# Performance work log

Measured on AMD Instinct MI355X. Metric: run time of the kernel, lower is better.

The kernel has to match this reference:

```python
import jax, jax.numpy as jnp
import numpy as np

DIM = 384
K = 64               # num_classes
TEMP = 0.1
BASE_TEMP = 2.0
LAMB = 25.0
PIXEL_SIZE = 50      # pixel_update_freq * 5
K_BAN = 10
SINKHORN_ITERS = 3
BS, N = 16, 512


def _l2norm(x, eps=1e-12):
    return x / jnp.maximum(jnp.linalg.norm(x, axis=-1, keepdims=True), eps)


def _online_clustering(scores):
    # SwAV-style Sinkhorn in log space on lamb-scaled cosine logits, then argmax.
    logq = scores
    for _ in range(SINKHORN_ITERS):
        logq = logq - jax.scipy.special.logsumexp(logq, axis=1, keepdims=True)
        logq = logq - jax.scipy.special.logsumexp(logq, axis=0, keepdims=True)
    return jnp.argmax(logq, axis=1)


def _supcon(anchor, y_anchor, contrast, y_contrast, exclude_diag, require_pos):
    # mask[i,j] = 1 if same label
    mask = (y_anchor[:, None] == y_contrast[None, :]).astype(anchor.dtype)
    logits = (anchor @ contrast.T) / TEMP
    logits = logits - jax.lax.stop_gradient(jnp.max(logits, axis=1, keepdims=True))
    if exclude_diag:
        mask = mask * (1.0 - jnp.eye(anchor.shape[0], dtype=anchor.dtype))
    exp_logits = jnp.exp(logits)
    # note: neg_mask = 1 - mask, so for exclude_diag the self term counts as negative (faithful)
    neg = (exp_logits * (1.0 - mask)).sum(axis=1, keepdims=True)
    log_prob = logits - jnp.log(exp_logits + neg)
    pos_cnt = mask.sum(axis=1)
    num = (mask * log_prob).sum(axis=1)
    if require_pos:
        valid = (pos_cnt > 0).astype(anchor.dtype)
        mlpp = jnp.where(pos_cnt > 0, num / jnp.maximum(pos_cnt, 1.0), 0.0)
        return -(TEMP / BASE_TEMP) * jnp.sum(mlpp) / jnp.maximum(valid.sum(), 1.0)
    return jnp.mean(-(TEMP / BASE_TEMP) * num / pos_cnt)


def _forward(feats, off_feats, cluster_center, point_queue):
    bs, n, dim = off_feats.shape
    n_off = _l2norm(off_feats.reshape(-1, dim))
    cluster_feats = jnp.concatenate([n_off, point_queue.reshape(-1, dim)], axis=0)
    log_alpha = cluster_feats @ cluster_center.T              # (bs*n + K*PIXEL_SIZE, K)
    labels = _online_clustering(log_alpha * LAMB)[: bs * n]
    f = _l2norm(feats).reshape(-1, dim)
    # ppc2: anchors vs sampled queue entries (same random column indices for every class)
    k_samp = PIXEL_SIZE - K_BAN
    idx = jax.random.permutation(jax.random.key(1), PIXEL_SIZE)[:k_samp]
    x_c = point_queue[:, idx, :].reshape(-1, dim)             # (K*k_samp, dim)
    y_c = jnp.repeat(jnp.arange(K), k_samp)
    loss = _supcon(f, labels, x_c, y_c, exclude_diag=False, require_pos=False)
    # ppc: anchors vs anchors, diagonal removed from positives
    loss = loss + _supcon(f, labels, f, labels, exclude_diag=True, require_pos=True)
    return loss


def setup_inputs() -> dict:
    key = jax.random.key(0)
    k1, k2, k3, k4 = jax.random.split(key, 4)
    feats = jax.random.normal(k1, (BS, N, DIM), dtype=jnp.float32)
    off_feats = jax.random.normal(k2, (BS, N, DIM), dtype=jnp.float32)
    cluster_center = _l2norm(jax.random.normal(k3, (K, DIM), dtype=jnp.float32))
    point_queue = _l2norm(jax.random.normal(k4, (K, PIXEL_SIZE, DIM), dtype=jnp.float32))
    return {"feats": feats, "off_feats": off_feats,
            "cluster_center": cluster_center, "point_queue": point_queue}


def reference(feats, off_feats, cluster_center, point_queue):
    return _forward(feats, off_feats, cluster_center, point_queue)
```

## Files before the change

### kernel.cpp

```cpp
#include <hip/hip_runtime.h>
#include <stdint.h>
#include <algorithm>

#define DIM   384
#define KCLS  64
#define NPIX  50
#define KSAMP 40
#define NANCH 8192
#define NQ    3200
#define NTOT  11392
#define NXC   2560

typedef __attribute__((ext_vector_type(8)))  short s16x8;
typedef __attribute__((ext_vector_type(16))) float f32x16;

struct Idx40 { int v[KSAMP]; };

__device__ __forceinline__ float wave_sum64(float v){
  #pragma unroll
  for (int o = 32; o >= 1; o >>= 1) v += __shfl_xor(v, o);
  return v;
}

__device__ __forceinline__ unsigned short f2bf(float x){
  union { float f; uint32_t u; } c; c.f = x;
  uint32_t r = c.u + 0x7FFFu + ((c.u >> 16) & 1u);
  if ((c.u & 0x7F800000u) == 0x7F800000u) r = c.u;
  return (unsigned short)(r >> 16);
}

__device__ __forceinline__ float bf2f(unsigned short h){
  union { uint32_t u; float f; } c; c.u = ((uint32_t)h) << 16;
  return c.f;
}

__device__ __forceinline__ void split_hl(float x, unsigned short& hi, unsigned short& lo){
  hi = f2bf(x);
  lo = f2bf(x - bf2f(hi));
}

__device__ __forceinline__ void gload16(const unsigned short* g, unsigned short* l){
  __builtin_amdgcn_global_load_lds(
      (const __attribute__((address_space(1))) unsigned int*)g,
      (__attribute__((address_space(3))) unsigned int*)l, 16, 0, 0);
}

__global__ __launch_bounds__(256) void norm_copy_k(const float* __restrict__ feats,
    const float* __restrict__ off, const float* __restrict__ pq,
    const float* __restrict__ CC,
    unsigned short* __restrict__ fNh,
    unsigned short* __restrict__ CFhi, unsigned short* __restrict__ CFlo,
    unsigned short* __restrict__ cchi, unsigned short* __restrict__ cclo,
    unsigned short* __restrict__ xch, Idx40 idx){
  int row  = blockIdx.x * 4 + (threadIdx.x >> 6);
  int lane = threadIdx.x & 63;
  if (row < 2 * NANCH){
    const float* src = (row < NANCH) ? feats + (size_t)row * DIM
                                     : off + (size_t)(row - NANCH) * DIM;
    float v[6]; float ss = 0.f;
    #pragma unroll
    for (int e = 0; e < 6; e++){ v[e] = src[lane + 64 * e]; ss += v[e] * v[e]; }
    ss = wave_sum64(ss);
    float inv = 1.f / fmaxf(sqrtf(ss), 1e-12f);
    if (row < NANCH){
      unsigned short* dh = fNh + (size_t)row * DIM;
      #pragma unroll
      for (int e = 0; e < 6; e++) dh[lane + 64 * e] = f2bf(v[e] * inv);
    } else {
      size_t base = (size_t)(row - NANCH) * DIM;
      #pragma unroll
      for (int e = 0; e < 6; e++){
        unsigned short h, l;
        split_hl(v[e] * inv, h, l);
        CFhi[base + lane + 64 * e] = h;
        CFlo[base + lane + 64 * e] = l;
      }
    }
  } else if (row < 2 * NANCH + NQ){
    int q = row - 2 * NANCH;
    const float* src = pq + (size_t)q * DIM;
    size_t base = (size_t)(NANCH + q) * DIM;
    #pragma unroll
    for (int e = 0; e < 6; e++){
      unsigned short h, l;
      split_hl(src[lane + 64 * e], h, l);
      CFhi[base + lane + 64 * e] = h;
      CFlo[base + lane + 64 * e] = l;
    }
  } else if (row < 2 * NANCH + NQ + KCLS){
    int r = row - 2 * NANCH - NQ;
    size_t base = (size_t)r * DIM;
    #pragma unroll
    for (int e = 0; e < 6; e++){
      unsigned short h, l;
      split_hl(CC[base + lane + 64 * e], h, l);
      cchi[base + lane + 64 * e] = h;
      cclo[base + lane + 64 * e] = l;
    }
  } else {
    int q = row - 2 * NANCH - NQ - KCLS;
    int c = q / KSAMP, t = q - c * KSAMP;
    const float* src = pq + ((size_t)c * NPIX + idx.v[t]) * DIM;
    unsigned short* dst = xch + (size_t)q * DIM;
    #pragma unroll
    for (int e = 0; e < 6; e++) dst[lane + 64 * e] = f2bf(src[lane + 64 * e]);
  }
}

__global__ __launch_bounds__(256) void gemm_logq_mfma_k(
    const unsigned short* __restrict__ Ahi, const unsigned short* __restrict__ Alo,
    const unsigned short* __restrict__ Bhi, const unsigned short* __restrict__ Blo,
    float* __restrict__ logq){
  __shared__ unsigned short lAh[128 * 64], lAl[128 * 64];
  __shared__ unsigned short lBh[64 * 64],  lBl[64 * 64];
  int t = threadIdx.x;
  int lane = t & 63, w = t >> 6;
  int l31 = lane & 31, half = lane >> 5;
  int i0 = blockIdx.x * 128;

  int rA = w * 32 + l31;
  int swA = ((rA & 7) << 4);
  int rB0 = l31, rB1 = 32 + l31;
  int swB = ((l31 & 7) << 4);

  f32x16 acc0, acc1;
  #pragma unroll
  for (int r = 0; r < 16; r++){ acc0[r] = 0.f; acc1[r] = 0.f; }

  for (int kc = 0; kc < 6; kc++){
    __syncthreads();
    #pragma unroll
    for (int p = 0; p < 4; p++){
      int c = t + p * 256;
      int row = c >> 3, col = c & 7;
      int sw = ((col << 4) ^ ((row & 7) << 4));
      *(s16x8*)((char*)lAh + row * 128 + sw) =
          *(const s16x8*)(Ahi + (size_t)(i0 + row) * DIM + kc * 64 + col * 8);
      *(s16x8*)((char*)lAl + row * 128 + sw) =
          *(const s16x8*)(Alo + (size_t)(i0 + row) * DIM + kc * 64 + col * 8);
    }
    #pragma unroll
    for (int p = 0; p < 2; p++){
      int c = t + p * 256;
      int row = c >> 3, col = c & 7;
      int sw = ((col << 4) ^ ((row & 7) << 4));
      *(s16x8*)((char*)lBh + row * 128 + sw) =
          *(const s16x8*)(Bhi + (size_t)row * DIM + kc * 64 + col * 8);
      *(s16x8*)((char*)lBl + row * 128 + sw) =
          *(const s16x8*)(Blo + (size_t)row * DIM + kc * 64 + col * 8);
    }
    __syncthreads();
    #pragma unroll
    for (int kk = 0; kk < 4; kk++){
      int kb = kk * 32 + half * 16;
      s16x8 fah  = *(const s16x8*)((char*)lAh + rA * 128 + (kb ^ swA));
      s16x8 fal  = *(const s16x8*)((char*)lAl + rA * 128 + (kb ^ swA));
      s16x8 fb0h = *(const s16x8*)((char*)lBh + rB0 * 128 + (kb ^ swB));
      s16x8 fb0l = *(const s16x8*)((char*)lBl + rB0 * 128 + (kb ^ swB));
      s16x8 fb1h = *(const s16x8*)((char*)lBh + rB1 * 128 + (kb ^ swB));
      s16x8 fb1l = *(const s16x8*)((char*)lBl + rB1 * 128 + (kb ^ swB));
      acc0 = __builtin_amdgcn_mfma_f32_32x32x16_bf16(fah, fb0h, acc0, 0, 0, 0);
      acc0 = __builtin_amdgcn_mfma_f32_32x32x16_bf16(fah, fb0l, acc0, 0, 0, 0);
      acc0 = __builtin_amdgcn_mfma_f32_32x32x16_bf16(fal, fb0h, acc0, 0, 0, 0);
      acc1 = __builtin_amdgcn_mfma_f32_32x32x16_bf16(fah, fb1h, acc1, 0, 0, 0);
      acc1 = __builtin_amdgcn_mfma_f32_32x32x16_bf16(fah, fb1l, acc1, 0, 0, 0);
      acc1 = __builtin_amdgcn_mfma_f32_32x32x16_bf16(fal, fb1h, acc1, 0, 0, 0);
    }
  }
  #pragma unroll
  for (int r = 0; r < 16; r++){
    int rowp = (r & 3) + 8 * (r >> 2) + 4 * half;
    size_t row = (size_t)(i0 + w * 32 + rowp);
    logq[row * KCLS + l31]      = 25.f * acc0[r];
    logq[row * KCLS + 32 + l31] = 25.f * acc1[r];
  }
}

__global__ __launch_bounds__(256) void rowpass_k(float* __restrict__ logq,
    const float* __restrict__ colsum, int useCol){
  int row  = blockIdx.x * 4 + (threadIdx.x >> 6);
  int lane = threadIdx.x & 63;
  float v = logq[(size_t)row * KCLS + lane];
  if (useCol) v -= logf(colsum[lane]);
  float m = v;
  #pragma unroll
  for (int o = 32; o >= 1; o >>= 1) m = fmaxf(m, __shfl_xor(m, o));
  float s = expf(v - m);
  s = wave_sum64(s);
  logq[(size_t)row * KCLS + lane] = v - (m + logf(s));
}

__global__ __launch_bounds__(256) void colsum_k(const float* __restrict__ logq,
    float* __restrict__ cs){
  int r0 = blockIdx.x * 128;
  int t = threadIdx.x, lane = t & 63, grp = t >> 6;
  float acc = 0.f;
  for (int r = grp; r < 128; r += 4)
    acc += __expf(logq[(size_t)(r0 + r) * KCLS + lane]);
  __shared__ float red[4][64];
  red[grp][lane] = acc;
  __syncthreads();
  if (t < 64) atomicAdd(&cs[t], red[0][t] + red[1][t] + red[2][t] + red[3][t]);
}

__global__ __launch_bounds__(256) void argmax_k(const float* __restrict__ logq,
    const float* __restrict__ cs, int* __restrict__ labels, int* __restrict__ cnt){
  __shared__ float clog[KCLS];
  int t = threadIdx.x;
  if (t < KCLS) clog[t] = logf(cs[t]);
  __syncthreads();
  int i = blockIdx.x * 256 + t;
  if (i >= NANCH) return;
  float best = -INFINITY; int bj = 0;
  for (int j = 0; j < KCLS; j++){
    float v = logq[(size_t)i * KCLS + j] - clog[j];
    if (v > best){ best = v; bj = j; }
  }
  labels[i] = bj;
  atomicAdd(&cnt[bj], 1);
}

__global__ void scan_k(const int* cnt, int* offs, int* offw){
  if (threadIdx.x == 0){
    int acc = 0;
    for (int c = 0; c < KCLS; c++){ offs[c] = acc; offw[c] = acc; acc += cnt[c]; }
  }
}

__global__ __launch_bounds__(256) void scatter_k(const int* __restrict__ labels,
    int* offw, int* __restrict__ sorted, const float* __restrict__ S,
    const float* __restrict__ S2, float* __restrict__ Sp, float* __restrict__ S2p){
  int i = blockIdx.x * 256 + threadIdx.x;
  if (i >= NANCH) return;
  int p = atomicAdd(&offw[labels[i]], 1);
  sorted[p] = i;
  Sp[p]  = S[i];
  S2p[p] = S2[i];
}

__global__ __launch_bounds__(256) void sortrows_k(const unsigned short* __restrict__ fNh,
    const int* __restrict__ sorted, unsigned short* __restrict__ fNs){
  int p = blockIdx.x * 4 + (threadIdx.x >> 6);
  int lane = threadIdx.x & 63;
  int src = sorted[p];
  const uint32_t* s = (const uint32_t*)(fNh + (size_t)src * DIM);
  uint32_t* d = (uint32_t*)(fNs + (size_t)p * DIM);
  #pragma unroll
  for (int e = 0; e < 3; e++) d[lane + 64 * e] = s[lane + 64 * e];
}

__global__ __launch_bounds__(256) void rowsums2_k(
    const unsigned short* __restrict__ A, const unsigned short* __restrict__ Bself,
    const unsigned short* __restrict__ Bxc, float* __restrict__ S, float* __restrict__ S2){
  __shared__ unsigned short lds[2][2][128 * 64];
  const unsigned short* Bp; float* dst; int jbase;
  if (blockIdx.y < 16){ Bp = Bself; dst = S;  jbase = blockIdx.y * 512; }
  else                { Bp = Bxc;   dst = S2; jbase = (blockIdx.y - 16) * 512; }

  int t = threadIdx.x, lane = t & 63, w = t >> 6;
  int wr = w >> 1, wc = w & 1;
  int l31 = lane & 31, half = lane >> 5;
  int i0 = blockIdx.x * 128;
  int lrow = lane >> 3, srcslot = (lane & 7) ^ lrow;
  size_t loff = (size_t)lrow * DIM + srcslot * 8;

  int rA0 = wr * 64 + l31, rA1 = rA0 + 32;
  int rB0 = wc * 64 + l31, rB1 = rB0 + 32;
  int swA = ((rA0 & 7) << 4), swB = ((rB0 & 7) << 4);

  f32x16 s0, s1, a00, a01, a10, a11;
  #pragma unroll
  for (int r = 0; r < 16; r++){ s0[r] = 0.f; s1[r] = 0.f; }

  #pragma unroll
  for (int c = 0; c < 4; c++){
    int chunk = w * 4 + c;
    gload16(A  + (size_t)(i0    + chunk * 8) * DIM + loff, &lds[0][0][chunk * 512]);
    gload16(Bp + (size_t)(jbase + chunk * 8) * DIM + loff, &lds[0][1][chunk * 512]);
  }
  __syncthreads();

  int buf = 0;
  for (int s = 0; s < 24; s++){
    int kc = s % 6;
    if (s < 23){
      int sn = s + 1;
      int jt1 = sn / 6, kc1 = sn - jt1 * 6;
      int j0 = jbase + jt1 * 128;
      int nb = buf ^ 1;
      #pragma unroll
      for (int c = 0; c < 4; c++){
        int chunk = w * 4 + c;
        gload16(A  + (size_t)(i0 + chunk * 8) * DIM + kc1 * 64 + loff, &lds[nb][0][chunk * 512]);
        gload16(Bp + (size_t)(j0 + chunk * 8) * DIM + kc1 * 64 + loff, &lds[nb][1][chunk * 512]);
      }
    }
    if (kc == 0){
      #pragma unroll
      for (int r = 0; r < 16; r++){ a00[r] = 0.f; a01[r] = 0.f; a10[r] = 0.f; a11[r] = 0.f; }
    }
    const char* bA = (const char*)&lds[buf][0][0];
    const char* bB = (const char*)&lds[buf][1][0];
    #pragma unroll
    for (int kk = 0; kk < 4; kk++){
      int kb = kk * 32 + half * 16;
      s16x8 fa0 = *(const s16x8*)(bA + rA0 * 128 + (kb ^ swA));
      s16x8 fa1 = *(const s16x8*)(bA + rA1 * 128 + (kb ^ swA));
      s16x8 fb0 = *(const s16x8*)(bB + rB0 * 128 + (kb ^ swB));
      s16x8 fb1 = *(const s16x8*)(bB + rB1 * 128 + (kb ^ swB));
      a00 = __builtin_amdgcn_mfma_f32_32x32x16_bf16(fa0, fb0, a00, 0, 0, 0);
      a01 = __builtin_amdgcn_mfma_f32_32x32x16_bf16(fa0, fb1, a01, 0, 0, 0);
      a10 = __builtin_amdgcn_mfma_f32_32x32x16_bf16(fa1, fb0, a10, 0, 0, 0);
      a11 = __builtin_amdgcn_mfma_f32_32x32x16_bf16(fa1, fb1, a11, 0, 0, 0);
    }
    if (kc == 5){
      #pragma unroll
      for (int r = 0; r < 16; r++){
        s0[r] += __expf(fmaf(a00[r], 10.f, -10.f)) + __expf(fmaf(a01[r], 10.f, -10.f));
        s1[r] += __expf(fmaf(a10[r], 10.f, -10.f)) + __expf(fmaf(a11[r], 10.f, -10.f));
      }
    }
    __syncthreads();
    buf ^= 1;
  }

  #pragma unroll
  for (int o = 1; o < 32; o <<= 1){
    #pragma unroll
    for (int r = 0; r < 16; r++){
      s0[r] += __shfl_xor(s0[r], o);
      s1[r] += __shfl_xor(s1[r], o);
    }
  }
  if (l31 == 0){
    #pragma unroll
    for (int r = 0; r < 16; r++){
      int rowp = (r & 3) + 8 * (r >> 2) + 4 * half;
      atomicAdd(&dst[i0 + wr * 64 + rowp], s0[r]);
      atomicAdd(&dst[i0 + wr * 64 + 32 + rowp], s1[r]);
    }
  }
}

__device__ __forceinline__ void gram2(const s16x8* afr,
    const unsigned short* b0, const unsigned short* b1, f32x16& acc0, f32x16& acc1){
  #pragma unroll
  for (int ks = 0; ks < 24; ks++){
    s16x8 v0 = *(const s16x8*)(b0 + ks * 16);
    s16x8 v1 = *(const s16x8*)(b1 + ks * 16);
    acc0 = __builtin_amdgcn_mfma_f32_32x32x16_bf16(afr[ks], v0, acc0, 0, 0, 0);
    acc1 = __builtin_amdgcn_mfma_f32_32x32x16_bf16(afr[ks], v1, acc1, 0, 0, 0);
  }
}

__global__ __launch_bounds__(64) void classpair_k(
    const unsigned short* __restrict__ fNs, const unsigned short* __restrict__ xch,
    const int* __restrict__ offs, const int* __restrict__ cnt,
    const float* __restrict__ S, const float* __restrict__ S2,
    float* __restrict__ num2A, float* __restrict__ mlppA, float* __restrict__ validA){
  int c = blockIdx.x;
  int n = cnt[c], o0 = offs[c];
  if (n == 0) return;
  int lane = threadIdx.x;
  int l31 = lane & 31, half = lane >> 5;
  int ntiles = (n + 31) >> 5;

  for (int rt = blockIdx.y; rt < ntiles; rt += gridDim.y){
    int rpos = rt * 32 + l31;
    const unsigned short* arow = fNs + (size_t)(o0 + (rpos < n ? rpos : 0)) * DIM + half * 8;
    s16x8 afr[24];
    #pragma unroll
    for (int ks = 0; ks < 24; ks++) afr[ks] = *(const s16x8*)(arow + ks * 16);

    f32x16 p20, p21;
    #pragma unroll
    for (int r = 0; r < 16; r++){ p20[r] = 0.f; p21[r] = 0.f; }
    {
      int c1 = 32 + l31;
      const unsigned short* b0 = xch + ((size_t)c * KSAMP + l31) * DIM + half * 8;
      const unsigned short* b1 = xch + ((size_t)c * KSAMP + (c1 < KSAMP ? c1 : 0)) * DIM + half * 8;
      gram2(afr, b0, b1, p20, p21);
    }
    f32x16 red;
    #pragma unroll
    for (int r = 0; r < 16; r++){
      float v0 = expf(fmaf(p20[r], 10.f, -10.f));
      float v1 = (l31 < 8) ? expf(fmaf(p21[r], 10.f, -10.f)) : 0.f;
      red[r] = v0 + v1;
    }
    #pragma unroll
    for (int o = 1; o < 32; o <<= 1)
      #pragma unroll
      for (int r = 0; r < 16; r++) red[r] += __shfl_xor(red[r], o);
    float neg2[16];
    #pragma unroll
    for (int r = 0; r < 16; r++){
      int rowp = (r & 3) + 8 * (r >> 2) + 4 * half;
      int rp = rt * 32 + rowp;
      neg2[r] = (rp < n) ? S2[o0 + rp] - red[r] : 1.f;
    }
    #pragma unroll
    for (int r = 0; r < 16; r++){
      float l0 = fmaf(p20[r], 10.f, -10.f);
      float l1 = fmaf(p21[r], 10.f, -10.f);
      float a = l0 - logf(expf(l0) + neg2[r]);
      float b = (l31 < 8) ? l1 - logf(expf(l1) + neg2[r]) : 0.f;
      red[r] = a + b;
    }
    #pragma unroll
    for (int o = 1; o < 32; o <<= 1)
      #pragma unroll
      for (int r = 0; r < 16; r++) red[r] += __shfl_xor(red[r], o);
    if (l31 == 0){
      #pragma unroll
      for (int r = 0; r < 16; r++){
        int rowp = (r & 3) + 8 * (r >> 2) + 4 * half;
        int rp = rt * 32 + rowp;
        if (rp < n) num2A[o0 + rp] = red[r];
      }
    }

    f32x16 pe;
    #pragma unroll
    for (int r = 0; r < 16; r++) pe[r] = 0.f;
    for (int ct = 0; ct < ntiles; ct += 2){
      int cp0 = ct * 32 + l31;
      int cp1 = (ct + 1) * 32 + l31;
      bool has1 = (ct + 1) < ntiles;
      const unsigned short* b0 = fNs + (size_t)(o0 + (cp0 < n ? cp0 : 0)) * DIM + half * 8;
      const unsigned short* b1 = fNs + (size_t)(o0 + (has1 && cp1 < n ? cp1 : 0)) * DIM + half * 8;
      f32x16 a0, a1;
      #pragma unroll
      for (int r = 0; r < 16; r++){ a0[r] = 0.f; a1[r] = 0.f; }
      gram2(afr, b0, b1, a0, a1);
      #pragma unroll
      for (int r = 0; r < 16; r++){
        int rowp = (r & 3) + 8 * (r >> 2) + 4 * half;
        int rp = rt * 32 + rowp;
        if (cp0 < n && cp0 != rp) pe[r] += expf(fmaf(a0[r], 10.f, -10.f));
        if (has1 && cp1 < n && cp1 != rp) pe[r] += expf(fmaf(a1[r], 10.f, -10.f));
      }
    }
    #pragma unroll
    for (int o = 1; o < 32; o <<= 1)
      #pragma unroll
      for (int r = 0; r < 16; r++) pe[r] += __shfl_xor(pe[r], o);
    float neg[16];
    #pragma unroll
    for (int r = 0; r < 16; r++){
      int rowp = (r & 3) + 8 * (r >> 2) + 4 * half;
      int rp = rt * 32 + rowp;
      neg[r] = (rp < n) ? S[o0 + rp] - pe[r] : 1.f;
    }

    f32x16 nm;
    #pragma unroll
    for (int r = 0; r < 16; r++) nm[r] = 0.f;
    for (int ct = 0; ct < ntiles; ct += 2){
      int cp0 = ct * 32 + l31;
      int cp1 = (ct + 1) * 32 + l31;
      bool has1 = (ct + 1) < ntiles;
      const unsigned short* b0 = fNs + (size_t)(o0 + (cp0 < n ? cp0 : 0)) * DIM + half * 8;
      const unsigned short* b1 = fNs + (size_t)(o0 + (has1 && cp1 < n ? cp1 : 0)) * DIM + half * 8;
      f32x16 a0, a1;
      #pragma unroll
      for (int r = 0; r < 16; r++){ a0[r] = 0.f; a1[r] = 0.f; }
      gram2(afr, b0, b1, a0, a1);
      #pragma unroll
      for (int r = 0; r < 16; r++){
        int rowp = (r & 3) + 8 * (r >> 2) + 4 * half;
        int rp = rt * 32 + rowp;
        if (cp0 < n && cp0 != rp){
          float l = fmaf(a0[r], 10.f, -10.f);
          nm[r] += l - logf(expf(l) + neg[r]);
        }
        if (has1 && cp1 < n && cp1 != rp){
          float l = fmaf(a1[r], 10.f, -10.f);
          nm[r] += l - logf(expf(l) + neg[r]);
        }
      }
    }
    #pragma unroll
    for (int o = 1; o < 32; o <<= 1)
      #pragma unroll
      for (int r = 0; r < 16; r++) nm[r] += __shfl_xor(nm[r], o);
    if (l31 == 0){
      #pragma unroll
      for (int r = 0; r < 16; r++){
        int rowp = (r & 3) + 8 * (r >> 2) + 4 * half;
        int rp = rt * 32 + rowp;
        if (rp < n){
          if (n > 1){ mlppA[o0 + rp] = nm[r] / (float)(n - 1); validA[o0 + rp] = 1.f; }
          else      { mlppA[o0 + rp] = 0.f; validA[o0 + rp] = 0.f; }
        }
      }
    }
  }
}

__global__ __launch_bounds__(256) void finalize_k(const float* __restrict__ num2A,
    const float* __restrict__ mlppA, const float* __restrict__ validA,
    float* __restrict__ out){
  int t = threadIdx.x;
  float s2 = 0.f, sm = 0.f, sv = 0.f;
  for (int i = t; i < NANCH; i += 256){ s2 += num2A[i]; sm += mlppA[i]; sv += validA[i]; }
  __shared__ float a2[256], am[256], av[256];
  a2[t] = s2; am[t] = sm; av[t] = sv; __syncthreads();
  for (int o = 128; o >= 1; o >>= 1){
    if (t < o){ a2[t] += a2[t+o]; am[t] += am[t+o]; av[t] += av[t+o]; }
    __syncthreads();
  }
  if (t == 0){
    float loss1 = -0.05f * a2[0] / (40.f * (float)NANCH);
    float loss2 = -0.05f * am[0] / fmaxf(av[0], 1.f);
    out[0] = loss1 + loss2;
  }
}

static void tf2x32(uint32_t k0, uint32_t k1, uint32_t x0, uint32_t x1, uint32_t out[2]){
  uint32_t ks[3] = { k0, k1, k0 ^ k1 ^ 0x1BD11BDAu };
  static const int R[2][4] = { {13,15,26,6}, {17,29,16,24} };
  x0 += ks[0]; x1 += ks[1];
  for (int i = 0; i < 5; i++){
    for (int j = 0; j < 4; j++){
      x0 += x1;
      int r = R[i & 1][j];
      x1 = (x1 << r) | (x1 >> (32 - r));
      x1 ^= x0;
    }
    x0 += ks[(i + 1) % 3];
    x1 += ks[(i + 2) % 3] + (uint32_t)(i + 1);
  }
  out[0] = x0; out[1] = x1;
}

static void compute_idx(int idx_out[KSAMP]){
  uint32_t p0[2], p1[2];
  tf2x32(0u, 1u, 0u, 2u, p0);
  tf2x32(0u, 1u, 1u, 3u, p1);
  uint32_t sk0 = p0[1], sk1 = p1[1];
  uint32_t bits[NPIX];
  for (int i = 0; i < 25; i++){
    uint32_t o[2];
    tf2x32(sk0, sk1, (uint32_t)i, (uint32_t)(25 + i), o);
    bits[i] = o[0]; bits[25 + i] = o[1];
  }
  int perm[NPIX];
  for (int i = 0; i < NPIX; i++) perm[i] = i;
  std::stable_sort(perm, perm + NPIX, [&](int a, int b){ return bits[a] < bits[b]; });
  for (int i = 0; i < KSAMP; i++) idx_out[i] = perm[i];
}

extern "C" void kernel_launch(void* const* d_in, const int* in_sizes, int n_in,
                              void* d_out, int out_size, void* d_ws, size_t ws_size,
                              hipStream_t stream){
  const float* feats = (const float*)d_in[0];
  const float* off   = (const float*)d_in[1];
  const float* cc    = (const float*)d_in[2];
  const float* pq    = (const float*)d_in[3];
  float* out = (float*)d_out;

  char* ws = (char*)d_ws;
  size_t ofs = 0;
  auto alloc = [&](size_t bytes) -> void* {
    ofs = (ofs + 255) & ~(size_t)255;
    void* p = ws + ofs;
    ofs += bytes;
    return p;
  };
  float* logq   = (float*)alloc((size_t)NTOT * KCLS * 4);
  unsigned short* fNh  = (unsigned short*)alloc((size_t)NANCH * DIM * 2);
  unsigned short* fNs  = (unsigned short*)alloc((size_t)NANCH * DIM * 2);
  unsigned short* CFhi = (unsigned short*)alloc((size_t)NTOT * DIM * 2);
  unsigned short* CFlo = (unsigned short*)alloc((size_t)NTOT * DIM * 2);
  unsigned short* cchi = (unsigned short*)alloc((size_t)KCLS * DIM * 2);
  unsigned short* cclo = (unsigned short*)alloc((size_t)KCLS * DIM * 2);
  unsigned short* xch  = (unsigned short*)alloc((size_t)NXC * DIM * 2);
  float* S2     = (float*)alloc((2 * NANCH + KCLS + 3 * KCLS) * 4);
  float* S      = S2 + NANCH;
  int*   cnt    = (int*)(S2 + 2 * NANCH);
  float* cs0    = S2 + 2 * NANCH + KCLS;
  float* cs1    = cs0 + KCLS;
  float* cs2    = cs1 + KCLS;
  float* Sp     = (float*)alloc(NANCH * 4);
  float* S2p    = (float*)alloc(NANCH * 4);
  float* num2A  = (float*)alloc(NANCH * 4);
  float* mlppA  = (float*)alloc(NANCH * 4);
  float* validA = (float*)alloc(NANCH * 4);
  int* labels   = (int*)alloc(NANCH * 4);
  int* sorted   = (int*)alloc(NANCH * 4);
  int* offs     = (int*)alloc(KCLS * 4);
  int* offw     = (int*)alloc(KCLS * 4);

  Idx40 idx;
  compute_idx(idx.v);

  hipMemsetAsync(S2, 0, (2 * NANCH + 4 * KCLS) * 4, stream);
  norm_copy_k<<<(2 * NANCH + NQ + KCLS + NXC) / 4, 256, 0, stream>>>(
      feats, off, pq, cc, fNh, CFhi, CFlo, cchi, cclo, xch, idx);
  rowsums2_k<<<dim3(64, 21), 256, 0, stream>>>(fNh, fNh, xch, S, S2);
  gemm_logq_mfma_k<<<NTOT / 128, 256, 0, stream>>>(CFhi, CFlo, cchi, cclo, logq);
  rowpass_k<<<NTOT / 4, 256, 0, stream>>>(logq, cs0, 0);
  colsum_k<<<NTOT / 128, 256, 0, stream>>>(logq, cs0);
  rowpass_k<<<NTOT / 4, 256, 0, stream>>>(logq, cs0, 1);
  colsum_k<<<NTOT / 128, 256, 0, stream>>>(logq, cs1);
  rowpass_k<<<NTOT / 4, 256, 0, stream>>>(logq, cs1, 1);
  colsum_k<<<NTOT / 128, 256, 0, stream>>>(logq, cs2);
  argmax_k<<<NANCH / 256, 256, 0, stream>>>(logq, cs2, labels, cnt);
  scan_k<<<1, 64, 0, stream>>>(cnt, offs, offw);
  scatter_k<<<NANCH / 256, 256, 0, stream>>>(labels, offw, sorted, S, S2, Sp, S2p);
  sortrows_k<<<NANCH / 4, 256, 0, stream>>>(fNh, sorted, fNs);
  classpair_k<<<dim3(KCLS, 8), 64, 0, stream>>>(fNs, xch, offs, cnt, Sp, S2p,
                                                num2A, mlppA, validA);
  finalize_k<<<1, 256, 0, stream>>>(num2A, mlppA, validA, out);
}
```

Baseline: 272.1 us.

## Exploit symmetry of anchor Gram matrix in rowsums kernel, computing upper triangle only

The self-similarity row-sum pass now computes only the block upper triangle of the symmetric anchor-anchor Gram matrix. Off-diagonal tiles add their exponentials to both the row sums and, through column reductions and atomicAdd, to the transposed rows. This roughly halves the MFMA and exp work for the self part. In exchange it adds atomics, gives uneven per-block work with early-exit blocks, and makes results depend on atomic ordering.

```diff
diff --git a/kernel.cpp b/kernel.cpp
--- a/kernel.cpp
+++ b/kernel.cpp
@@ -252,15 +252,26 @@
 __global__ __launch_bounds__(256) void rowsums2_k(
     const unsigned short* __restrict__ A, const unsigned short* __restrict__ Bself,
     const unsigned short* __restrict__ Bxc, float* __restrict__ S, float* __restrict__ S2){
+  int bi = blockIdx.x;
+  const unsigned short* Bp; float* dst;
+  int bj0, njt; bool selfpart;
+  if (blockIdx.y < 16){
+    selfpart = true; Bp = Bself; dst = S;
+    bj0 = bi + (int)blockIdx.y * 4;
+    njt = 64 - bj0;
+    if (njt <= 0) return;
+    if (njt > 4) njt = 4;
+  } else {
+    selfpart = false; Bp = Bxc; dst = S2;
+    bj0 = ((int)blockIdx.y - 16) * 4;
+    njt = 4;
+  }
+
   __shared__ unsigned short lds[2][2][128 * 64];
-  const unsigned short* Bp; float* dst; int jbase;
-  if (blockIdx.y < 16){ Bp = Bself; dst = S;  jbase = blockIdx.y * 512; }
-  else                { Bp = Bxc;   dst = S2; jbase = (blockIdx.y - 16) * 512; }
-
   int t = threadIdx.x, lane = t & 63, w = t >> 6;
   int wr = w >> 1, wc = w & 1;
   int l31 = lane & 31, half = lane >> 5;
-  int i0 = blockIdx.x * 128;
+  int i0 = bi * 128;
   int lrow = lane >> 3, srcslot = (lane & 7) ^ lrow;
   size_t loff = (size_t)lrow * DIM + srcslot * 8;
 
@@ -275,24 +286,25 @@
   #pragma unroll
   for (int c = 0; c < 4; c++){
     int chunk = w * 4 + c;
-    gload16(A  + (size_t)(i0    + chunk * 8) * DIM + loff, &lds[0][0][chunk * 512]);
-    gload16(Bp + (size_t)(jbase + chunk * 8) * DIM + loff, &lds[0][1][chunk * 512]);
+    gload16(A  + (size_t)(i0         + chunk * 8) * DIM + loff, &lds[0][0][chunk * 512]);
+    gload16(Bp + (size_t)(bj0 * 128  + chunk * 8) * DIM + loff, &lds[0][1][chunk * 512]);
   }
   __syncthreads();
 
+  int total = njt * 6;
   int buf = 0;
-  for (int s = 0; s < 24; s++){
-    int kc = s % 6;
-    if (s < 23){
+  for (int s = 0; s < total; s++){
+    int jt = s / 6, kc = s - jt * 6;
+    if (s + 1 < total){
       int sn = s + 1;
       int jt1 = sn / 6, kc1 = sn - jt1 * 6;
-      int j0 = jbase + jt1 * 128;
+      int j1 = (bj0 + jt1) * 128;
       int nb = buf ^ 1;
       #pragma unroll
       for (int c = 0; c < 4; c++){
         int chunk = w * 4 + c;
         gload16(A  + (size_t)(i0 + chunk * 8) * DIM + kc1 * 64 + loff, &lds[nb][0][chunk * 512]);
-        gload16(Bp + (size_t)(j0 + chunk * 8) * DIM + kc1 * 64 + loff, &lds[nb][1][chunk * 512]);
+        gload16(Bp + (size_t)(j1 + chunk * 8) * DIM + kc1 * 64 + loff, &lds[nb][1][chunk * 512]);
       }
     }
     if (kc == 0){
@@ -314,10 +326,27 @@
       a11 = __builtin_amdgcn_mfma_f32_32x32x16_bf16(fa1, fb1, a11, 0, 0, 0);
     }
     if (kc == 5){
+      int j0 = (bj0 + jt) * 128;
+      bool docol = selfpart && (bj0 + jt != bi);
+      float c0 = 0.f, c1 = 0.f;
       #pragma unroll
       for (int r = 0; r < 16; r++){
-        s0[r] += __expf(fmaf(a00[r], 10.f, -10.f)) + __expf(fmaf(a01[r], 10.f, -10.f));
-        s1[r] += __expf(fmaf(a10[r], 10.f, -10.f)) + __expf(fmaf(a11[r], 10.f, -10.f));
+        float e00 = __expf(fmaf(a00[r], 10.f, -10.f));
+        float e01 = __expf(fmaf(a01[r], 10.f, -10.f));
+        float e10 = __expf(fmaf(a10[r], 10.f, -10.f));
+        float e11 = __expf(fmaf(a11[r], 10.f, -10.f));
+        s0[r] += e00 + e01;
+        s1[r] += e10 + e11;
+        c0 += e00 + e10;
+        c1 += e01 + e11;
+      }
+      if (docol){
+        c0 += __shfl_xor(c0, 32);
+        c1 += __shfl_xor(c1, 32);
+        if (half == 0){
+          atomicAdd(&dst[j0 + wc * 64 + l31], c0);
+          atomicAdd(&dst[j0 + wc * 64 + 32 + l31], c1);
+        }
       }
     }
     __syncthreads();
```

Result: faster. 252.6 us (-7.2%).
